# Performance work log

Measured on AMD Instinct MI355X. Metric: run time of the kernel, lower is better.

Reference implementation:

```python
import jax, jax.numpy as jnp
import numpy as np

B, S, D, H = 2, 2048, 1024, 16
HD = D // H  # head_dim = 64
NEG_INF = -jnp.inf


def _rope_tables(seq_len, head_dim, theta=10000.0):
    inv = 1.0 / (theta ** (np.arange(0, head_dim, 2, dtype=np.float32) / head_dim))
    t = np.arange(seq_len, dtype=np.float32)
    ang = np.outer(t, inv)  # [S, HD/2]
    return jnp.asarray(np.cos(ang)), jnp.asarray(np.sin(ang))


def _apply_rope(x, cos, sin):
    # x: [B, S, H, HD]; pairs (even, odd) rotated by complex freqs, matching
    # torch.view_as_complex(reshape(..., -1, 2)) * freqs_cis.
    x2 = x.reshape(*x.shape[:-1], HD // 2, 2)
    x0, x1 = x2[..., 0], x2[..., 1]
    c = cos[None, :, None, :]
    s = sin[None, :, None, :]
    o0 = x0 * c - x1 * s
    o1 = x0 * s + x1 * c
    return jnp.stack([o0, o1], axis=-1).reshape(x.shape)


def setup_inputs() -> dict:
    key = jax.random.key(0)
    ks = jax.random.split(key, 10)
    sc = 1.0 / np.sqrt(D)
    return {
        "x": jax.random.normal(ks[0], (B, S, D), dtype=jnp.float32),
        "effective_len": jax.random.randint(ks[1], (B,), 0, 1024, dtype=jnp.int32),
        "Wq": jax.random.normal(ks[2], (D, D), dtype=jnp.float32) * sc,
        "bq": jnp.zeros((D,), dtype=jnp.float32),
        "Wk": jax.random.normal(ks[3], (D, D), dtype=jnp.float32) * sc,
        "bk": jnp.zeros((D,), dtype=jnp.float32),
        "Wv": jax.random.normal(ks[4], (D, D), dtype=jnp.float32) * sc,
        "bv": jnp.zeros((D,), dtype=jnp.float32),
        "Wo": jax.random.normal(ks[5], (D, D), dtype=jnp.float32) * sc,
        "bo": jnp.zeros((D,), dtype=jnp.float32),
    }


def reference(x, effective_len, Wq, bq, Wk, bk, Wv, bv, Wo, bo):
    cos, sin = _rope_tables(S, HD)
    q = (x @ Wq.T + bq).reshape(B, S, H, HD)
    k = (x @ Wk.T + bk).reshape(B, S, H, HD)
    v = (x @ Wv.T + bv).reshape(B, S, H, HD)
    q = _apply_rope(q, cos, sin)
    k = _apply_rope(k, cos, sin)
    # [B, H, S, S]
    scores = jnp.einsum("bqhd,bkhd->bhqk", q, k) / np.sqrt(HD)
    row = jnp.arange(S)[:, None]
    col = jnp.arange(S)[None, :]
    causal = jnp.where(col > row, NEG_INF, 0.0)  # [S, S]
    scores = scores + causal[None, None, :, :]
    # faithful replication of original: masks the LAST effective_len key columns
    pad = jnp.where(col[None, 0, :] >= (S - effective_len)[:, None], NEG_INF, 0.0)  # [B, S]
    scores = scores + pad[:, None, None, :]
    probs = jax.nn.softmax(scores.astype(jnp.float32), axis=-1).astype(x.dtype)
    out = jnp.einsum("bhqk,bkhd->bqhd", probs, v).reshape(B, S, D)
    return out @ Wo.T + bo  # dropout in eval mode = identity
```

## Files before the change

### kernel.cpp

```cpp
#include <hip/hip_runtime.h>

#define SB   2048
#define DD   1024
#define NH   16
#define HDIM 64
#define NB   2

typedef float f4 __attribute__((ext_vector_type(4)));
typedef __bf16 bf16x8 __attribute__((ext_vector_type(8)));
typedef unsigned short u16;
typedef unsigned int u32;
typedef unsigned long long u64;
typedef u16 u16x8 __attribute__((ext_vector_type(8)));
typedef u16 u16x4 __attribute__((ext_vector_type(4)));

#define QSCALE 0.1803368801111f

__device__ __forceinline__ u16 f2bf(float f) {
  unsigned u = __float_as_uint(f);
  u += 0x7FFFu + ((u >> 16) & 1u);
  return (u16)(u >> 16);
}

typedef __attribute__((address_space(3))) unsigned int lds_uint;
typedef __attribute__((address_space(1))) const unsigned int glb_uint;
__device__ __forceinline__ void gl_lds16(const void* g, void* l) {
  __builtin_amdgcn_global_load_lds((glb_uint*)g, (lds_uint*)l, 16, 0, 0);
}

__device__ __forceinline__ void cvt8(const float* __restrict__ src,
                                     u16* __restrict__ dst, size_t i) {
  f4 a = *(const f4*)(src + 8 * i);
  f4 b = *(const f4*)(src + 8 * i + 4);
  u16x8 o;
  o[0] = f2bf(a[0]); o[1] = f2bf(a[1]); o[2] = f2bf(a[2]); o[3] = f2bf(a[3]);
  o[4] = f2bf(b[0]); o[5] = f2bf(b[1]); o[6] = f2bf(b[2]); o[7] = f2bf(b[3]);
  *(u16x8*)(dst + 8 * i) = o;
}

__global__ __launch_bounds__(256) void prep_kernel(
    const float* __restrict__ x, const float* __restrict__ Wq,
    const float* __restrict__ Wk, const float* __restrict__ Wv,
    u16* __restrict__ xb, u16* __restrict__ Wb3,
    float* __restrict__ cosT, float* __restrict__ sinT) {
  int bid = blockIdx.x, t = threadIdx.x;
  if (bid < 2048) {
    cvt8(x, xb, (size_t)bid * 256 + t);
  } else if (bid < 2560) {
    cvt8(Wq, Wb3, (size_t)(bid - 2048) * 256 + t);
  } else if (bid < 3072) {
    cvt8(Wk, Wb3 + (1u << 20), (size_t)(bid - 2560) * 256 + t);
  } else if (bid < 3584) {
    cvt8(Wv, Wb3 + (2u << 20), (size_t)(bid - 3072) * 256 + t);
  } else {
    int idx = (bid - 3584) * 256 + t;
    int tt = idx & 31, s = idx >> 5;
    float inv = powf(10000.0f, -2.0f * (float)tt / 64.0f);
    float ang = (float)s * inv;
    cosT[idx] = cosf(ang);
    sinT[idx] = sinf(ang);
  }
}

__global__ __launch_bounds__(256) void cvt_bf16_kernel(const float* __restrict__ src,
                                                       u16* __restrict__ dst) {
  cvt8(src, dst, (size_t)blockIdx.x * 256 + threadIdx.x);
}

__global__ __launch_bounds__(256) void gemm_qkv_fused_kernel(
    const u16* __restrict__ A, const u16* __restrict__ W3,
    const float* __restrict__ bq, const float* __restrict__ bk,
    const float* __restrict__ bv,
    u16* __restrict__ Qw, u16* __restrict__ Kw, u16* __restrict__ Vt,
    const float* __restrict__ cosT, const float* __restrict__ sinT) {
  const int K = DD;
  __shared__ u16 As[128 * 64];
  __shared__ u16 Bs[128 * 64];
  const int t = threadIdx.x;
  const int wave = t >> 6, lane = t & 63;
  const int m0 = blockIdx.x * 128, n0 = blockIdx.y * 128;
  const int mw = (wave >> 1) * 64, nw = (wave & 1) * 64;
  const int quad = lane >> 4, l15 = lane & 15;
  const int srow = lane >> 3, sgran = lane & 7;
  const u16* Ab = A + (size_t)m0 * K;
  const u16* Bb = W3 + (size_t)n0 * K;
  f4 acc[4][4];
#pragma unroll
  for (int i = 0; i < 4; i++)
#pragma unroll
    for (int j = 0; j < 4; j++) acc[i][j] = (f4)0.f;

  for (int kt = 0; kt < K; kt += 64) {
#pragma unroll
    for (int is = 0; is < 4; is++) {
      int r = wave * 32 + is * 8 + srow;
      int lg = sgran ^ (r & 7);
      gl_lds16(Ab + (size_t)r * K + kt + lg * 8, &As[(wave * 32 + is * 8) * 64]);
      gl_lds16(Bb + (size_t)r * K + kt + lg * 8, &Bs[(wave * 32 + is * 8) * 64]);
    }
    __syncthreads();
#pragma unroll
    for (int kh = 0; kh < 2; kh++) {
      bf16x8 af[4], bfr[4];
#pragma unroll
      for (int i = 0; i < 4; i++) {
        int R = mw + 16 * i + l15;
        af[i] = *(const bf16x8*)&As[R * 64 + ((kh * 4 + quad) ^ (R & 7)) * 8];
        int Rb = nw + 16 * i + l15;
        bfr[i] = *(const bf16x8*)&Bs[Rb * 64 + ((kh * 4 + quad) ^ (Rb & 7)) * 8];
      }
#pragma unroll
      for (int i = 0; i < 4; i++)
#pragma unroll
        for (int j = 0; j < 4; j++)
          acc[i][j] = __builtin_amdgcn_mfma_f32_16x16x32_bf16(af[i], bfr[j],
                                                              acc[i][j], 0, 0, 0);
    }
    __syncthreads();
  }

#pragma unroll
  for (int j = 0; j < 4; j++) {
    int colg3 = n0 + nw + 16 * j + l15;
    int which = colg3 >> 10;
    int c = colg3 & 1023;
    int h = c >> 6, dh = c & 63, tt2 = dh >> 1;
    float bval = (which == 0 ? bq : which == 1 ? bk : bv)[c];
    if (which == 2) {
#pragma unroll
      for (int i = 0; i < 4; i++) {
        int mg0 = m0 + mw + 16 * i + quad * 4;
        int b = mg0 >> 11, sr0 = mg0 & (SB - 1);
        u16x4 pk4;
#pragma unroll
        for (int r = 0; r < 4; r++) pk4[r] = f2bf(acc[i][j][r] + bval);
        *(u16x4*)(Vt + ((size_t)(b * NH + h) * HDIM + dh) * SB + sr0) = pk4;
      }
    } else {
      u16* dst = which ? Kw : Qw;
      float scale = which ? 1.0f : QSCALE;
#pragma unroll
      for (int i = 0; i < 4; i++)
#pragma unroll
        for (int r = 0; r < 4; r++) {
          int mg = m0 + mw + 16 * i + quad * 4 + r;
          int b = mg >> 11, sr = mg & (SB - 1);
          float v = acc[i][j][r] + bval;
          float vp = __shfl_xor(v, 1);
          float cc = cosT[sr * 32 + tt2], ss = sinT[sr * 32 + tt2];
          v = ((lane & 1) == 0) ? (v * cc - vp * ss) : (vp * ss + v * cc);
          dst[(((size_t)(b * NH + h)) * SB + sr) * HDIM + dh] = f2bf(v * scale);
        }
    }
  }
}

__global__ __launch_bounds__(256) void gemm_out_kernel(
    const u16* __restrict__ A, const u16* __restrict__ W,
    const float* __restrict__ bias, float* __restrict__ outp) {
  const int K = DD;
  __shared__ u16 As[128 * 64];
  __shared__ u16 Bs[64 * 64];
  const int t = threadIdx.x;
  const int wave = t >> 6, lane = t & 63;
  const int m0 = blockIdx.x * 128, n0 = blockIdx.y * 64;
  const int mw = (wave >> 1) * 64, nw = (wave & 1) * 32;
  const int quad = lane >> 4, l15 = lane & 15;
  const int srow = lane >> 3, sgran = lane & 7;
  const u16* Ab = A + (size_t)m0 * K;
  const u16* Bb = W + (size_t)n0 * K;
  f4 acc[4][2];
#pragma unroll
  for (int i = 0; i < 4; i++)
#pragma unroll
    for (int j = 0; j < 2; j++) acc[i][j] = (f4)0.f;

  for (int kt = 0; kt < K; kt += 64) {
#pragma unroll
    for (int is = 0; is < 4; is++) {
      int r = wave * 32 + is * 8 + srow;
      int lg = sgran ^ (r & 7);
      gl_lds16(Ab + (size_t)r * K + kt + lg * 8, &As[(wave * 32 + is * 8) * 64]);
    }
#pragma unroll
    for (int is = 0; is < 2; is++) {
      int r = wave * 16 + is * 8 + srow;
      int lg = sgran ^ (r & 7);
      gl_lds16(Bb + (size_t)r * K + kt + lg * 8, &Bs[(wave * 16 + is * 8) * 64]);
    }
    __syncthreads();
#pragma unroll
    for (int kh = 0; kh < 2; kh++) {
      bf16x8 af[4], bfr[2];
#pragma unroll
      for (int i = 0; i < 4; i++) {
        int R = mw + 16 * i + l15;
        af[i] = *(const bf16x8*)&As[R * 64 + ((kh * 4 + quad) ^ (R & 7)) * 8];
      }
#pragma unroll
      for (int j = 0; j < 2; j++) {
        int R = nw + 16 * j + l15;
        bfr[j] = *(const bf16x8*)&Bs[R * 64 + ((kh * 4 + quad) ^ (R & 7)) * 8];
      }
#pragma unroll
      for (int i = 0; i < 4; i++)
#pragma unroll
        for (int j = 0; j < 2; j++)
          acc[i][j] = __builtin_amdgcn_mfma_f32_16x16x32_bf16(af[i], bfr[j],
                                                              acc[i][j], 0, 0, 0);
    }
    __syncthreads();
  }
#pragma unroll
  for (int i = 0; i < 4; i++)
#pragma unroll
    for (int j = 0; j < 2; j++) {
      int colg = n0 + nw + 16 * j + l15;
#pragma unroll
      for (int r = 0; r < 4; r++) {
        int mg = m0 + mw + 16 * i + quad * 4 + r;
        outp[(size_t)mg * DD + colg] = acc[i][j][r] + bias[colg];
      }
    }
}

__global__ __launch_bounds__(512) void attn_mfma_kernel(
    const u16* __restrict__ Qw, const u16* __restrict__ Kw,
    const u16* __restrict__ Vt, u16* __restrict__ Ow,
    const int* __restrict__ eff) {
  __shared__ u16 KL[2][8 * 64 * 8];
  __shared__ u16 VL[2][8 * 64 * 8];
  const int w = threadIdx.x >> 6, lane = threadIdx.x & 63;
  const int l15 = lane & 15, q4 = lane >> 4;
  const int qp = blockIdx.x;
  const int wg = w >> 2, wl = w & 3;
  const int QT = wg ? (SB / 128 - 1 - qp) : qp;
  const int h = blockIdx.y, b = blockIdx.z;
  const int limit = SB - eff[b];
  const size_t bh = ((size_t)b * NH + h) * (SB * HDIM);

  const int rowbase = QT * 128 + wl * 32;

  bf16x8 qf[2][2];
  {
    const u16* qp0 = Qw + bh + (size_t)(rowbase + l15) * HDIM + q4 * 8;
    qf[0][0] = *(const bf16x8*)qp0;
    qf[0][1] = *(const bf16x8*)(qp0 + 32);
    const u16* qp1 = qp0 + 16 * HDIM;
    qf[1][0] = *(const bf16x8*)qp1;
    qf[1][1] = *(const bf16x8*)(qp1 + 32);
  }

  f4 acc[2][4];
#pragma unroll
  for (int s = 0; s < 2; s++)
#pragma unroll
    for (int dt = 0; dt < 4; dt++) acc[s][dt] = (f4)0.f;
  float l_run[2] = {0.f, 0.f};

  const int kendB = min((SB / 128 - 1 - qp) * 128 + 127, limit - 1);
  const int ntiles = (kendB >> 6) + 1;
  const int wkend = min(rowbase + 31, limit - 1);

#define STAGE_TILE(TILE, BUF)                                                   \
  {                                                                             \
    const int colb_ = (TILE) * 64;                                              \
    _Pragma("unroll") for (int f = 0; f < 2; f++) {                             \
      int fr = w * 2 + f;                                                       \
      if (fr < 8) {                                                             \
        int mt = fr >> 1, j = fr & 1;                                           \
        gl_lds16(Kw + bh + (size_t)(colb_ + mt * 16 + l15) * HDIM + q4 * 8 + j * 32, \
                 &KL[BUF][fr * 512]);                                           \
      } else {                                                                  \
        int fv = fr - 8, dt = fv >> 1, j = fv & 1;                              \
        gl_lds16(Vt + bh + (size_t)(dt * 16 + l15) * SB + colb_ + q4 * 8 + j * 32, \
                 &VL[BUF][fv * 512]);                                           \
      }                                                                         \
    }                                                                           \
  }

  STAGE_TILE(0, 0)
  __syncthreads();

  for (int kt = 0; kt < ntiles; kt++) {
    const int cur = kt & 1;
    const int colb = kt * 64;
    if (kt + 1 < ntiles) STAGE_TILE(kt + 1, cur ^ 1)

    if (colb <= wkend) {
      f4 sa[2][4];
#pragma unroll
      for (int mt = 0; mt < 4; mt++) {
        bf16x8 k0 = *(const bf16x8*)&KL[cur][(mt * 2 + 0) * 512 + lane * 8];
        bf16x8 k1 = *(const bf16x8*)&KL[cur][(mt * 2 + 1) * 512 + lane * 8];
        f4 s0 = (f4)0.f, s1 = (f4)0.f;
        s0 = __builtin_amdgcn_mfma_f32_16x16x32_bf16(k0, qf[0][0], s0, 0, 0, 0);
        s0 = __builtin_amdgcn_mfma_f32_16x16x32_bf16(k1, qf[0][1], s0, 0, 0, 0);
        s1 = __builtin_amdgcn_mfma_f32_16x16x32_bf16(k0, qf[1][0], s1, 0, 0, 0);
        s1 = __builtin_amdgcn_mfma_f32_16x16x32_bf16(k1, qf[1][1], s1, 0, 0, 0);
        sa[0][mt] = s0;
        sa[1][mt] = s1;
      }

      u32 pk[2][4][2];
#pragma unroll
      for (int s = 0; s < 2; s++) {
        const int rb = rowbase + 16 * s;
        const int rg = rb + l15;
        const bool needmask = (colb + 63 > rb) || (colb + 63 >= limit);
        if (needmask) {
#pragma unroll
          for (int mt = 0; mt < 4; mt++)
#pragma unroll
            for (int r = 0; r < 4; r++) {
              int col = colb + mt * 16 + q4 * 4 + r;
              if (col > rg || col >= limit) sa[s][mt][r] = -3.0e38f;
            }
        }
        float lsum = 0.f;
#pragma unroll
        for (int mt = 0; mt < 4; mt++) {
          float p0 = exp2f(sa[s][mt][0]);
          float p1 = exp2f(sa[s][mt][1]);
          float p2 = exp2f(sa[s][mt][2]);
          float p3 = exp2f(sa[s][mt][3]);
          lsum += (p0 + p1) + (p2 + p3);
          pk[s][mt][0] = (__float_as_uint(p1) & 0xFFFF0000u) | (__float_as_uint(p0) >> 16);
          pk[s][mt][1] = (__float_as_uint(p3) & 0xFFFF0000u) | (__float_as_uint(p2) >> 16);
        }
        l_run[s] += lsum;
      }

      const int srcA = ((q4 & 1) << 5) + l15;
      const int hi = q4 >> 1;
#pragma unroll
      for (int s = 0; s < 2; s++) {
        union { u32 wds[4]; bf16x8 v; } ub0, ub1;
#pragma unroll
        for (int d = 0; d < 4; d++) {
          int src = srcA + ((d >> 1) << 4);
          u32 t0 = (u32)__shfl((int)pk[s][0][d & 1], src);
          u32 t1 = (u32)__shfl((int)pk[s][1][d & 1], src);
          ub0.wds[d] = hi ? t1 : t0;
          u32 t2 = (u32)__shfl((int)pk[s][2][d & 1], src);
          u32 t3 = (u32)__shfl((int)pk[s][3][d & 1], src);
          ub1.wds[d] = hi ? t3 : t2;
        }
#pragma unroll
        for (int dt = 0; dt < 4; dt++) {
          bf16x8 v0 = *(const bf16x8*)&VL[cur][(dt * 2 + 0) * 512 + lane * 8];
          bf16x8 v1 = *(const bf16x8*)&VL[cur][(dt * 2 + 1) * 512 + lane * 8];
          acc[s][dt] = __builtin_amdgcn_mfma_f32_16x16x32_bf16(v0, ub0.v, acc[s][dt], 0, 0, 0);
          acc[s][dt] = __builtin_amdgcn_mfma_f32_16x16x32_bf16(v1, ub1.v, acc[s][dt], 0, 0, 0);
        }
      }
    }
    __syncthreads();
  }

#pragma unroll
  for (int s = 0; s < 2; s++) {
    float lt = l_run[s];
    lt += __shfl_xor(lt, 16);
    lt += __shfl_xor(lt, 32);
    const float linv = 1.0f / lt;
    const int rg = rowbase + 16 * s + l15;
    const size_t obase = (((size_t)b * SB + rg) * NH + h) * HDIM + q4 * 4;
#pragma unroll
    for (int dt = 0; dt < 4; dt++) {
      u16x4 o;
      o[0] = f2bf(acc[s][dt][0] * linv);
      o[1] = f2bf(acc[s][dt][1] * linv);
      o[2] = f2bf(acc[s][dt][2] * linv);
      o[3] = f2bf(acc[s][dt][3] * linv);
      *(u16x4*)(Ow + obase + dt * 16) = o;
    }
  }
}

extern "C" void kernel_launch(void* const* d_in, const int* in_sizes, int n_in,
                              void* d_out, int out_size, void* d_ws, size_t ws_size,
                              hipStream_t stream) {
  (void)in_sizes; (void)n_in; (void)out_size; (void)ws_size;
  const float* x  = (const float*)d_in[0];
  const int*   eff = (const int*)d_in[1];
  const float* Wq = (const float*)d_in[2];
  const float* bq = (const float*)d_in[3];
  const float* Wk = (const float*)d_in[4];
  const float* bk = (const float*)d_in[5];
  const float* Wv = (const float*)d_in[6];
  const float* bv = (const float*)d_in[7];
  const float* Wo = (const float*)d_in[8];
  const float* bo = (const float*)d_in[9];
  float* out = (float*)d_out;

  char* ws = (char*)d_ws;
  u16* Qw = (u16*)(ws);
  u16* Kw = (u16*)(ws + (8u << 20));
  u16* Vt = (u16*)(ws + (16u << 20));
  u16* Ow = (u16*)(ws + (24u << 20));
  u16* xb = (u16*)(ws + (24u << 20));
  u16* Wb3 = (u16*)(ws + (32u << 20));
  float* cosT = (float*)(ws + (38u << 20));
  float* sinT = (float*)(ws + (38u << 20) + (256u << 10));

  hipLaunchKernelGGL(prep_kernel, dim3(3840), dim3(256), 0, stream,
                     x, Wq, Wk, Wv, xb, Wb3, cosT, sinT);

  hipLaunchKernelGGL(gemm_qkv_fused_kernel, dim3(32, 24), dim3(256), 0, stream,
                     xb, Wb3, bq, bk, bv, Qw, Kw, Vt, cosT, sinT);

  hipLaunchKernelGGL(cvt_bf16_kernel, dim3(512), dim3(256), 0, stream, Wo, Wb3);

  hipLaunchKernelGGL(attn_mfma_kernel, dim3(SB / 256, NH, NB), dim3(512), 0, stream,
                     Qw, Kw, Vt, Ow, eff);

  hipLaunchKernelGGL(gemm_out_kernel, dim3(32, 16), dim3(256), 0, stream, Ow, Wb3, bo, out);
}
```

Before: 202.1 us.

## Split attention key range across two wave groups and fold Wo conversion into prep

The attention kernel now runs 1024 threads per block. Two halves of the block process alternating 64-key tiles with separate double-buffered LDS. Their partial output accumulators and row sums are combined through LDS at the end, which raises wave-level parallelism per query tile for the skewed causal work. Separately, the Wo fp32-to-bf16 conversion moves into the prep kernel, removing one launch. The costs are an extra reduction step with block barriers, and the occupancy and register limits that come with 1024-thread blocks.

New measurement: 205.0 us. No clear change (+1.4%).

```diff
diff --git a/kernel.cpp b/kernel.cpp
--- a/kernel.cpp
+++ b/kernel.cpp
@@ -41,7 +41,8 @@
 __global__ __launch_bounds__(256) void prep_kernel(
     const float* __restrict__ x, const float* __restrict__ Wq,
     const float* __restrict__ Wk, const float* __restrict__ Wv,
-    u16* __restrict__ xb, u16* __restrict__ Wb3,
+    const float* __restrict__ Wo,
+    u16* __restrict__ xb, u16* __restrict__ Wb3, u16* __restrict__ Wob,
     float* __restrict__ cosT, float* __restrict__ sinT) {
   int bid = blockIdx.x, t = threadIdx.x;
   if (bid < 2048) {
@@ -52,19 +53,16 @@
     cvt8(Wk, Wb3 + (1u << 20), (size_t)(bid - 2560) * 256 + t);
   } else if (bid < 3584) {
     cvt8(Wv, Wb3 + (2u << 20), (size_t)(bid - 3072) * 256 + t);
+  } else if (bid < 4096) {
+    cvt8(Wo, Wob, (size_t)(bid - 3584) * 256 + t);
   } else {
-    int idx = (bid - 3584) * 256 + t;
+    int idx = (bid - 4096) * 256 + t;
     int tt = idx & 31, s = idx >> 5;
     float inv = powf(10000.0f, -2.0f * (float)tt / 64.0f);
     float ang = (float)s * inv;
     cosT[idx] = cosf(ang);
     sinT[idx] = sinf(ang);
   }
-}
-
-__global__ __launch_bounds__(256) void cvt_bf16_kernel(const float* __restrict__ src,
-                                                       u16* __restrict__ dst) {
-  cvt8(src, dst, (size_t)blockIdx.x * 256 + threadIdx.x);
 }
 
 __global__ __launch_bounds__(256) void gemm_qkv_fused_kernel(
@@ -224,16 +222,17 @@
     }
 }
 
-__global__ __launch_bounds__(512) void attn_mfma_kernel(
+__global__ __launch_bounds__(1024) void attn_mfma_kernel(
     const u16* __restrict__ Qw, const u16* __restrict__ Kw,
     const u16* __restrict__ Vt, u16* __restrict__ Ow,
     const int* __restrict__ eff) {
-  __shared__ u16 KL[2][8 * 64 * 8];
-  __shared__ u16 VL[2][8 * 64 * 8];
+  __shared__ u16 SMEM[2][2][2][4096];
   const int w = threadIdx.x >> 6, lane = threadIdx.x & 63;
   const int l15 = lane & 15, q4 = lane >> 4;
+  const int kh2 = w >> 3;
+  const int wr = w & 7;
+  const int wg = wr >> 2, wl = wr & 3;
   const int qp = blockIdx.x;
-  const int wg = w >> 2, wl = w & 3;
   const int QT = wg ? (SB / 128 - 1 - qp) : qp;
   const int h = blockIdx.y, b = blockIdx.z;
   const int limit = SB - eff[b];
@@ -260,39 +259,42 @@
 
   const int kendB = min((SB / 128 - 1 - qp) * 128 + 127, limit - 1);
   const int ntiles = (kendB >> 6) + 1;
+  const int ntmax = (ntiles + 1) >> 1;
   const int wkend = min(rowbase + 31, limit - 1);
 
 #define STAGE_TILE(TILE, BUF)                                                   \
   {                                                                             \
     const int colb_ = (TILE) * 64;                                              \
     _Pragma("unroll") for (int f = 0; f < 2; f++) {                             \
-      int fr = w * 2 + f;                                                       \
+      int fr = wr * 2 + f;                                                      \
       if (fr < 8) {                                                             \
         int mt = fr >> 1, j = fr & 1;                                           \
         gl_lds16(Kw + bh + (size_t)(colb_ + mt * 16 + l15) * HDIM + q4 * 8 + j * 32, \
-                 &KL[BUF][fr * 512]);                                           \
+                 &SMEM[0][kh2][BUF][fr * 512]);                                 \
       } else {                                                                  \
         int fv = fr - 8, dt = fv >> 1, j = fv & 1;                              \
         gl_lds16(Vt + bh + (size_t)(dt * 16 + l15) * SB + colb_ + q4 * 8 + j * 32, \
-                 &VL[BUF][fv * 512]);                                           \
+                 &SMEM[1][kh2][BUF][fv * 512]);                                 \
       }                                                                         \
     }                                                                           \
   }
 
-  STAGE_TILE(0, 0)
+  STAGE_TILE(kh2, 0)
   __syncthreads();
 
-  for (int kt = 0; kt < ntiles; kt++) {
-    const int cur = kt & 1;
+  for (int i = 0; i < ntmax; i++) {
+    const int kt = 2 * i + kh2;
+    const int cur = i & 1;
     const int colb = kt * 64;
-    if (kt + 1 < ntiles) STAGE_TILE(kt + 1, cur ^ 1)
-
-    if (colb <= wkend) {
+    const bool have = (kt < ntiles);
+    if (kt + 2 < ntiles) STAGE_TILE(kt + 2, cur ^ 1)
+
+    if (have && colb <= wkend) {
       f4 sa[2][4];
 #pragma unroll
       for (int mt = 0; mt < 4; mt++) {
-        bf16x8 k0 = *(const bf16x8*)&KL[cur][(mt * 2 + 0) * 512 + lane * 8];
-        bf16x8 k1 = *(const bf16x8*)&KL[cur][(mt * 2 + 1) * 512 + lane * 8];
+        bf16x8 k0 = *(const bf16x8*)&SMEM[0][kh2][cur][(mt * 2 + 0) * 512 + lane * 8];
+        bf16x8 k1 = *(const bf16x8*)&SMEM[0][kh2][cur][(mt * 2 + 1) * 512 + lane * 8];
         f4 s0 = (f4)0.f, s1 = (f4)0.f;
         s0 = __builtin_amdgcn_mfma_f32_16x16x32_bf16(k0, qf[0][0], s0, 0, 0, 0);
         s0 = __builtin_amdgcn_mfma_f32_16x16x32_bf16(k1, qf[0][1], s0, 0, 0, 0);
@@ -348,8 +350,8 @@
         }
 #pragma unroll
         for (int dt = 0; dt < 4; dt++) {
-          bf16x8 v0 = *(const bf16x8*)&VL[cur][(dt * 2 + 0) * 512 + lane * 8];
-          bf16x8 v1 = *(const bf16x8*)&VL[cur][(dt * 2 + 1) * 512 + lane * 8];
+          bf16x8 v0 = *(const bf16x8*)&SMEM[1][kh2][cur][(dt * 2 + 0) * 512 + lane * 8];
+          bf16x8 v1 = *(const bf16x8*)&SMEM[1][kh2][cur][(dt * 2 + 1) * 512 + lane * 8];
           acc[s][dt] = __builtin_amdgcn_mfma_f32_16x16x32_bf16(v0, ub0.v, acc[s][dt], 0, 0, 0);
           acc[s][dt] = __builtin_amdgcn_mfma_f32_16x16x32_bf16(v1, ub1.v, acc[s][dt], 0, 0, 0);
         }
@@ -358,22 +360,46 @@
     __syncthreads();
   }
 
+  float* XCH = (float*)&SMEM[0][0][0][0];
+  const int xidx = (wr * 64 + lane) * 17;
 #pragma unroll
   for (int s = 0; s < 2; s++) {
-    float lt = l_run[s];
-    lt += __shfl_xor(lt, 16);
-    lt += __shfl_xor(lt, 32);
-    const float linv = 1.0f / lt;
-    const int rg = rowbase + 16 * s + l15;
-    const size_t obase = (((size_t)b * SB + rg) * NH + h) * HDIM + q4 * 4;
-#pragma unroll
-    for (int dt = 0; dt < 4; dt++) {
-      u16x4 o;
-      o[0] = f2bf(acc[s][dt][0] * linv);
-      o[1] = f2bf(acc[s][dt][1] * linv);
-      o[2] = f2bf(acc[s][dt][2] * linv);
-      o[3] = f2bf(acc[s][dt][3] * linv);
-      *(u16x4*)(Ow + obase + dt * 16) = o;
+    if (kh2 == 1) {
+#pragma unroll
+      for (int dt = 0; dt < 4; dt++)
+#pragma unroll
+        for (int r = 0; r < 4; r++) XCH[xidx + dt * 4 + r] = acc[s][dt][r];
+      XCH[xidx + 16] = l_run[s];
+    }
+    __syncthreads();
+    if (kh2 == 0) {
+#pragma unroll
+      for (int dt = 0; dt < 4; dt++)
+#pragma unroll
+        for (int r = 0; r < 4; r++) acc[s][dt][r] += XCH[xidx + dt * 4 + r];
+      l_run[s] += XCH[xidx + 16];
+    }
+    __syncthreads();
+  }
+
+  if (kh2 == 0) {
+#pragma unroll
+    for (int s = 0; s < 2; s++) {
+      float lt = l_run[s];
+      lt += __shfl_xor(lt, 16);
+      lt += __shfl_xor(lt, 32);
+      const float linv = 1.0f / lt;
+      const int rg = rowbase + 16 * s + l15;
+      const size_t obase = (((size_t)b * SB + rg) * NH + h) * HDIM + q4 * 4;
+#pragma unroll
+      for (int dt = 0; dt < 4; dt++) {
+        u16x4 o;
+        o[0] = f2bf(acc[s][dt][0] * linv);
+        o[1] = f2bf(acc[s][dt][1] * linv);
+        o[2] = f2bf(acc[s][dt][2] * linv);
+        o[3] = f2bf(acc[s][dt][3] * linv);
+        *(u16x4*)(Ow + obase + dt * 16) = o;
+      }
     }
   }
 }
@@ -401,19 +427,18 @@
   u16* Ow = (u16*)(ws + (24u << 20));
   u16* xb = (u16*)(ws + (24u << 20));
   u16* Wb3 = (u16*)(ws + (32u << 20));
-  float* cosT = (float*)(ws + (38u << 20));
-  float* sinT = (float*)(ws + (38u << 20) + (256u << 10));
-
-  hipLaunchKernelGGL(prep_kernel, dim3(3840), dim3(256), 0, stream,
-                     x, Wq, Wk, Wv, xb, Wb3, cosT, sinT);
+  u16* Wob = (u16*)(ws + (38u << 20));
+  float* cosT = (float*)(ws + (40u << 20));
+  float* sinT = (float*)(ws + (40u << 20) + (256u << 10));
+
+  hipLaunchKernelGGL(prep_kernel, dim3(4352), dim3(256), 0, stream,
+                     x, Wq, Wk, Wv, Wo, xb, Wb3, Wob, cosT, sinT);
 
   hipLaunchKernelGGL(gemm_qkv_fused_kernel, dim3(32, 24), dim3(256), 0, stream,
                      xb, Wb3, bq, bk, bv, Qw, Kw, Vt, cosT, sinT);
 
-  hipLaunchKernelGGL(cvt_bf16_kernel, dim3(512), dim3(256), 0, stream, Wo, Wb3);
-
-  hipLaunchKernelGGL(attn_mfma_kernel, dim3(SB / 256, NH, NB), dim3(512), 0, stream,
+  hipLaunchKernelGGL(attn_mfma_kernel, dim3(SB / 256, NH, NB), dim3(1024), 0, stream,
                      Qw, Kw, Vt, Ow, eff);
 
-  hipLaunchKernelGGL(gemm_out_kernel, dim3(32, 16), dim3(256), 0, stream, Ow, Wb3, bo, out);
-}
+  hipLaunchKernelGGL(gemm_out_kernel, dim3(32, 16), dim3(256), 0, stream, Ow, Wob, bo, out);
+}
```
